# Performance work log

Measured on AMD Instinct MI355X. Metric: run time of the kernel, lower is better.

## Reference

```python
import jax, jax.numpy as jnp
import numpy as np

B, S, IN, OUT, H, M = 16, 512, 512, 512, 8, 4
HF = OUT // H  # head_feats = 64


def setup_inputs() -> dict:
    key = jax.random.key(0)
    ks = jax.random.split(key, 12)
    std = 0.02
    queries = jax.random.normal(ks[0], (B, S, IN), jnp.float32)
    keys = jax.random.normal(ks[1], (B, S, IN), jnp.float32)
    timespans = jax.random.uniform(ks[2], (B, S), jnp.float32)
    # causal mask tiled over heads*batch, matching [H*B, S, S] score shape
    attention_masks = jnp.broadcast_to(jnp.tril(jnp.ones((S, S), jnp.float32)), (H * B, S, S))
    event_marks = jax.random.uniform(ks[3], (H * B, 1, S, M), jnp.float32)
    Wq = std * jax.random.normal(ks[4], (IN, OUT), jnp.float32)
    Wk = std * jax.random.normal(ks[5], (IN, OUT), jnp.float32)
    Wv = std * jax.random.normal(ks[6], (IN, OUT), jnp.float32)
    Wt = std * jax.random.normal(ks[7], (IN, OUT), jnp.float32)
    Wi = std * jax.random.normal(ks[8], (HF + 1, M * HF), jnp.float32)  # fc_i weight
    bi = jnp.zeros((M * HF,), jnp.float32)                               # fc_i bias
    weight_i = std * jax.random.normal(ks[9], (M, HF), jnp.float32)
    scale_i = jnp.zeros((M,), jnp.float32)
    return {"queries": queries, "keys": keys, "timespans": timespans,
            "attention_masks": attention_masks, "event_marks": event_marks,
            "Wq": Wq, "Wk": Wk, "Wv": Wv, "Wt": Wt, "Wi": Wi, "bi": bi,
            "weight_i": weight_i, "scale_i": scale_i}


def reference(queries, keys, timespans, attention_masks, event_marks,
              Wq, Wk, Wv, Wt, Wi, bi, weight_i, scale_i):
    # torch's cat(chunk(X, H, dim=2), dim=0) == [B,S,H,HF] -> [H,B,S,HF] -> flat h*B+b
    def split_heads(X):
        return X.reshape(B, S, H, HF).transpose(2, 0, 1, 3)  # [H,B,S,HF]

    Q = split_heads(queries @ Wq)
    K = split_heads(keys @ Wk)
    V = split_heads(keys @ Wv)
    T = split_heads(keys @ Wt)

    scores = jnp.einsum('hbqf,hbkf->hbqk', Q, K) / jnp.sqrt(jnp.float32(OUT))
    mask = attention_masks.reshape(H, B, S, S)
    scores = jnp.where(mask == 0.0, jnp.float32(-2 ** 32 + 1), scores)
    attn = jax.nn.softmax(scores, axis=-1)  # [H,B,Sq,Sk]

    E = jnp.einsum('hbqk,hbkf->hbqf', attn, T)  # events fed to intensity net

    # --- Hawkes intensities ---
    ts = jnp.broadcast_to(timespans[None, :, :, None], (H, B, S, 1))
    mu = jax.nn.sigmoid(jnp.concatenate([E, ts], axis=-1) @ Wi + bi)  # [H,B,S,M*HF]
    mu = mu.reshape(H, B, S, M, HF)  # chunk over marks along feature dim
    scale = jnp.exp(scale_i)  # [M]
    lam = jnp.einsum('hbsmf,mf->hbsm', mu, weight_i) / scale
    lam = scale * jnp.log1p(jnp.exp(lam))  # scaled softplus, [H,B,S,M]

    # mark_inty[h,b,q,k] = sum_m lam[h,b,q,m] * event_marks[h,b,k,m]
    em = event_marks.reshape(H, B, S, M)
    mark_inty = jnp.einsum('hbqm,hbkm->hbqk', lam, em)

    out = jnp.einsum('hbqk,hbkf->hbqf', attn * mark_inty, V)
    out = out.transpose(1, 2, 0, 3).reshape(B, S, OUT) + queries[..., :OUT]
    all_mark_inty = lam.reshape(H * B, S, M)
    return out, all_mark_inty
```

## Files before the change

kernel.cpp:

```cpp
#include <hip/hip_runtime.h>
#include <math.h>

typedef __attribute__((ext_vector_type(8))) short short8;
typedef __attribute__((ext_vector_type(4))) float f32x4;

static __device__ __forceinline__ unsigned short f2bf(float f) {
  unsigned int u = __float_as_uint(f);
  u += 0x7FFFu + ((u >> 16) & 1u);
  return (unsigned short)(u >> 16);
}

static __device__ __forceinline__ void cp16(void* lds, const void* g) {
  __builtin_amdgcn_global_load_lds((const __attribute__((address_space(1))) void*)g,
                                   (__attribute__((address_space(3))) void*)lds,
                                   16, 0, 0);
}

__global__ __launch_bounds__(256) void convert_k(
    const float* __restrict__ qin, const float* __restrict__ kin,
    const float* __restrict__ Wq, const float* __restrict__ Wk,
    const float* __restrict__ Wv, const float* __restrict__ Wt,
    const float* __restrict__ Wi,
    unsigned short* __restrict__ qbf, unsigned short* __restrict__ kbf,
    unsigned short* __restrict__ Wb, unsigned short* __restrict__ WiF)
{
  __shared__ unsigned short tr[64 * 68];
  const int blk = blockIdx.x, tid = threadIdx.x;
  if (blk < 8192) {
    const float* src = (blk < 4096) ? qin : kin;
    unsigned short* dst = (blk < 4096) ? qbf : kbf;
    int i = ((blk & 4095) * 256 + tid) * 4;
    float4 v = *(const float4*)(src + i);
    ushort4 o;
    o.x = f2bf(v.x); o.y = f2bf(v.y); o.z = f2bf(v.z); o.w = f2bf(v.w);
    *(ushort4*)(dst + i) = o;
  } else if (blk < 8448) {
    int t = blk - 8192;
    int which = t >> 6, tile = t & 63;
    int r0 = (tile >> 3) << 6, c0 = (tile & 7) << 6;
    const float* W = (which == 0) ? Wq : (which == 1) ? Wk : (which == 2) ? Wv : Wt;
    const int rr = tid >> 4, cc = (tid & 15) << 2;
#pragma unroll
    for (int u = 0; u < 4; ++u) {
      int r = rr + u * 16;
      float4 v = *(const float4*)(W + (size_t)(r0 + r) * 512 + c0 + cc);
      tr[(cc + 0) * 68 + r] = f2bf(v.x);
      tr[(cc + 1) * 68 + r] = f2bf(v.y);
      tr[(cc + 2) * 68 + r] = f2bf(v.z);
      tr[(cc + 3) * 68 + r] = f2bf(v.w);
    }
    __syncthreads();
    unsigned short* dst = Wb + which * 262144;
#pragma unroll
    for (int u = 0; u < 4; ++u) {
      int c = rr + u * 16;
      ushort4 o = *(const ushort4*)&tr[c * 68 + cc];
      *(ushort4*)(dst + (size_t)(c0 + c) * 512 + r0 + cc) = o;
    }
  } else {
    int e = (blk - 8448) * 256 + tid;
    int j = e & 7, ll = (e >> 3) & 63, r = e >> 9;
    int kk = r % 3, nt = r / 3;
    int col = nt * 16 + (ll & 15);
    int k = kk * 32 + (ll >> 4) * 8 + j;
    float val = (k < 64) ? Wi[k * 256 + col] : ((k == 64) ? Wi[16384 + col] : 0.0f);
    WiF[e] = f2bf(val);
  }
}

__global__ __launch_bounds__(256) void proj_mfma(
    const unsigned short* __restrict__ qin_bf, const unsigned short* __restrict__ kin_bf,
    const unsigned short* __restrict__ Wb,
    unsigned short* __restrict__ Qg, unsigned short* __restrict__ Kg,
    unsigned short* __restrict__ Vt, unsigned short* __restrict__ Tt)
{
  const int which = blockIdx.z;
  const unsigned short* A = (which == 0) ? qin_bf : kin_bf;
  const unsigned short* W = Wb + which * 262144;
  const int row0 = blockIdx.x * 128;
  const int col0 = blockIdx.y * 128;
  const int tid = threadIdx.x;
  const int wv = tid >> 6, l = tid & 63;
  const int quad = l >> 4, lc = l & 15;
  const int wm = wv >> 1, wn = wv & 1;

  __shared__ unsigned short Asm[128 * 32];
  __shared__ unsigned short Bsm[128 * 32];

  f32x4 acc[4][4] = {};
  const int c0 = tid, c1 = tid + 256;

  for (int k0 = 0; k0 < 512; k0 += 32) {
    __syncthreads();
    cp16(&Asm[c0 * 8], A + (size_t)(row0 + (c0 >> 2)) * 512 + k0 + (c0 & 3) * 8);
    cp16(&Asm[c1 * 8], A + (size_t)(row0 + (c1 >> 2)) * 512 + k0 + (c1 & 3) * 8);
    cp16(&Bsm[c0 * 8], W + (size_t)(col0 + (c0 >> 2)) * 512 + k0 + (c0 & 3) * 8);
    cp16(&Bsm[c1 * 8], W + (size_t)(col0 + (c1 >> 2)) * 512 + k0 + (c1 & 3) * 8);
    __syncthreads();
    short8 a[4], b[4];
#pragma unroll
    for (int mi = 0; mi < 4; ++mi)
      a[mi] = *(const short8*)&Asm[(wm * 64 + mi * 16 + lc) * 32 + quad * 8];
#pragma unroll
    for (int nj = 0; nj < 4; ++nj)
      b[nj] = *(const short8*)&Bsm[(wn * 64 + nj * 16 + lc) * 32 + quad * 8];
#pragma unroll
    for (int mi = 0; mi < 4; ++mi)
#pragma unroll
      for (int nj = 0; nj < 4; ++nj)
        acc[mi][nj] = __builtin_amdgcn_mfma_f32_16x16x32_bf16(a[mi], b[nj], acc[mi][nj], 0, 0, 0);
  }

  const int h = (col0 >> 6) + wn;
  const int bidx = row0 >> 9;
  const int hb = h * 16 + bidx;
  if (which < 2) {
    unsigned short* C = (which == 0) ? Qg : Kg;
#pragma unroll
    for (int mi = 0; mi < 4; ++mi) {
      int sbase = (row0 & 511) + wm * 64 + mi * 16 + quad * 4;
#pragma unroll
      for (int nj = 0; nj < 4; ++nj) {
        size_t base = (size_t)hb * 32768 + (size_t)sbase * 64 + nj * 16 + lc;
#pragma unroll
        for (int reg = 0; reg < 4; ++reg)
          C[base + (size_t)reg * 64] = f2bf(acc[mi][nj][reg]);
      }
    }
  } else {
    unsigned short* C = (which == 2) ? Vt : Tt;
    unsigned short* scr = wn ? Bsm : Asm;
    const int sb = (row0 & 511) + wm * 64;
    __syncthreads();
#pragma unroll
    for (int round = 0; round < 2; ++round) {
      if (wm == round) {
#pragma unroll
        for (int mi = 0; mi < 4; ++mi)
#pragma unroll
          for (int nj = 0; nj < 4; ++nj)
#pragma unroll
            for (int reg = 0; reg < 4; ++reg) {
              int f = nj * 16 + lc, s = mi * 16 + quad * 4 + reg;
              int g = (s >> 3) ^ (f & 7);
              scr[f * 64 + g * 8 + (s & 7)] = f2bf(acc[mi][nj][reg]);
            }
#pragma unroll
        for (int it = 0; it < 8; ++it) {
          int fl = it * 8 + (l >> 3);
          int gg = (l & 7) ^ (fl & 7);
          short8 v = *(const short8*)&scr[fl * 64 + gg * 8];
          *(short8*)(C + (size_t)hb * 32768 + (size_t)fl * 512 + sb + (l & 7) * 8) = v;
        }
      }
      __syncthreads();
    }
  }
}

__global__ __launch_bounds__(256, 3) void attn_fused(
    const unsigned short* __restrict__ Qg, const unsigned short* __restrict__ Kg,
    const unsigned short* __restrict__ Vtg, const unsigned short* __restrict__ Ttg,
    const unsigned short* __restrict__ WiF,
    const float* __restrict__ bi, const float* __restrict__ wim,
    const float* __restrict__ sci, const float* __restrict__ tsp,
    const float* __restrict__ em, const float* __restrict__ queries,
    float* __restrict__ out, float* __restrict__ lamout)
{
  const int hb = blockIdx.y;
  const int qt = 7 - blockIdx.x;
  const int q0 = qt << 6;
  const int tid = threadIdx.x, wv = tid >> 6, l = tid & 63;
  const int quad = l >> 4, lc = l & 15;
  const int xg = lc & 7;

  __shared__ unsigned short Qs[4096];
  __shared__ unsigned short Ks[4096];
  __shared__ unsigned short TVs[4096];
  __shared__ unsigned short Wl[4][1536];
  __shared__ float emS[256];

  const int e1 = tid + 256;
  const int sr0 = tid >> 3, sg0 = (tid & 7) ^ (sr0 & 7);
  const int sr1 = e1 >> 3,  sg1 = (e1 & 7) ^ (sr1 & 7);
  const int sqk0 = sr0 * 64 + sg0 * 8,  sqk1 = sr1 * 64 + sg1 * 8;
  const int stv0 = sr0 * 512 + sg0 * 8, stv1 = sr1 * 512 + sg1 * 8;

  const float scl = 0.044194173824159216f;
  const int gqbase = q0 + wv * 16 + quad * 4;

  const unsigned short* Qbase = Qg + (size_t)hb * 32768 + q0 * 64;
  cp16(&Qs[tid * 8], Qbase + sqk0);
  cp16(&Qs[e1 * 8], Qbase + sqk1);

  f32x4 Eacc[4] = {};
  float lsum[4] = {0.f, 0.f, 0.f, 0.f};

  for (int kt = 0; kt <= qt; ++kt) {
    const int k0 = kt << 6;
    __syncthreads();
    const unsigned short* Kbase = Kg + (size_t)hb * 32768 + k0 * 64;
    cp16(&Ks[tid * 8], Kbase + sqk0);
    cp16(&Ks[e1 * 8], Kbase + sqk1);
    const unsigned short* Tbase = Ttg + (size_t)hb * 32768 + k0;
    cp16(&TVs[tid * 8], Tbase + stv0);
    cp16(&TVs[e1 * 8], Tbase + stv1);
    __syncthreads();

    f32x4 sc[4] = {};
#pragma unroll
    for (int kk = 0; kk < 2; ++kk) {
      short8 a = *(const short8*)&Qs[(wv * 16 + lc) * 64 + ((kk * 4 + quad) ^ xg) * 8];
#pragma unroll
      for (int nj = 0; nj < 4; ++nj) {
        short8 b = *(const short8*)&Ks[(nj * 16 + lc) * 64 + ((kk * 4 + quad) ^ xg) * 8];
        sc[nj] = __builtin_amdgcn_mfma_f32_16x16x32_bf16(a, b, sc[nj], 0, 0, 0);
      }
    }
    const bool diag = (kt == qt);
#pragma unroll
    for (int nj = 0; nj < 4; ++nj) {
      int col = nj * 16 + lc;
#pragma unroll
      for (int reg = 0; reg < 4; ++reg) {
        float pv = __expf(sc[nj][reg] * scl);
        if (diag && (k0 + col) > (gqbase + reg)) pv = 0.0f;
        lsum[reg] += pv;
        int row = quad * 4 + reg;
        int gp = (nj * 2 + (lc >> 3)) ^ (row & 7);
        Wl[wv][row * 96 + gp * 8 + (lc & 7)] = f2bf(pv);
      }
    }
#pragma unroll
    for (int kk = 0; kk < 2; ++kk) {
      short8 a = *(const short8*)&Wl[wv][lc * 96 + ((kk * 4 + quad) ^ xg) * 8];
#pragma unroll
      for (int fj = 0; fj < 4; ++fj) {
        short8 b = *(const short8*)&TVs[(fj * 16 + lc) * 64 + ((kk * 4 + quad) ^ xg) * 8];
        Eacc[fj] = __builtin_amdgcn_mfma_f32_16x16x32_bf16(a, b, Eacc[fj], 0, 0, 0);
      }
    }
  }

  float inv[4];
#pragma unroll
  for (int reg = 0; reg < 4; ++reg) {
    float s = lsum[reg];
#pragma unroll
    for (int off = 1; off < 16; off <<= 1) s += __shfl_xor(s, off);
    inv[reg] = 1.0f / s;
  }

#pragma unroll
  for (int reg = 0; reg < 4; ++reg) {
    int row = quad * 4 + reg;
    unsigned short* rp = &Wl[wv][row * 96];
#pragma unroll
    for (int fj = 0; fj < 4; ++fj) {
      int gp = (fj * 2 + (lc >> 3)) ^ (row & 7);
      rp[gp * 8 + (lc & 7)] = f2bf(Eacc[fj][reg] * inv[reg]);
    }
    float tsv = (lc == 0) ? tsp[(hb & 15) * 512 + gqbase + reg] : 0.0f;
    int gt = 8 + ((lc >> 3) ^ (row & 3));
    rp[gt * 8 + (lc & 7)] = f2bf(tsv);
    int gz = 8 + ((2 + (lc >> 3)) ^ (row & 3));
    rp[gz * 8 + (lc & 7)] = 0;
  }

  short8 ia[3];
  ia[0] = *(const short8*)&Wl[wv][lc * 96 + ((0 + quad) ^ xg) * 8];
  ia[1] = *(const short8*)&Wl[wv][lc * 96 + ((4 + quad) ^ xg) * 8];
  ia[2] = *(const short8*)&Wl[wv][lc * 96 + (8 + (quad ^ (lc & 3))) * 8];
  float lam4[4][4] = {};
#pragma unroll
  for (int nt = 0; nt < 16; ++nt) {
    f32x4 iacc = {};
#pragma unroll
    for (int kk = 0; kk < 3; ++kk) {
      short8 b = *(const short8*)(WiF + ((nt * 3 + kk) * 64 + l) * 8);
      iacc = __builtin_amdgcn_mfma_f32_16x16x32_bf16(ia[kk], b, iacc, 0, 0, 0);
    }
    float bvv = bi[nt * 16 + lc];
    float wmv = wim[nt * 16 + lc];
#pragma unroll
    for (int reg = 0; reg < 4; ++reg) {
      float mu = 1.0f / (1.0f + __expf(-(iacc[reg] + bvv)));
      lam4[reg][nt >> 2] += mu * wmv;
    }
  }
#pragma unroll
  for (int m = 0; m < 4; ++m) {
    float scv = __expf(sci[m]);
#pragma unroll
    for (int reg = 0; reg < 4; ++reg) {
      float s = lam4[reg][m];
#pragma unroll
      for (int off = 1; off < 16; off <<= 1) s += __shfl_xor(s, off);
      float z = s / scv;
      float sp = (z > 20.0f) ? z : log1pf(__expf(z));
      lam4[reg][m] = scv * sp;
    }
  }
  if (lc < 4) {
#pragma unroll
    for (int reg = 0; reg < 4; ++reg) {
      float v = (lc == 0) ? lam4[reg][0] : (lc == 1) ? lam4[reg][1]
              : (lc == 2) ? lam4[reg][2] : lam4[reg][3];
      lamout[((size_t)hb * 512 + gqbase + reg) * 4 + lc] = v;
    }
  }

  f32x4 Oacc[4] = {};
  for (int kt = 0; kt <= qt; ++kt) {
    const int k0 = kt << 6;
    __syncthreads();
    const unsigned short* Kbase = Kg + (size_t)hb * 32768 + k0 * 64;
    cp16(&Ks[tid * 8], Kbase + sqk0);
    cp16(&Ks[e1 * 8], Kbase + sqk1);
    const unsigned short* Vbase = Vtg + (size_t)hb * 32768 + k0;
    cp16(&TVs[tid * 8], Vbase + stv0);
    cp16(&TVs[e1 * 8], Vbase + stv1);
    emS[tid] = em[(size_t)hb * 2048 + k0 * 4 + tid];
    __syncthreads();

    f32x4 sc[4] = {};
#pragma unroll
    for (int kk = 0; kk < 2; ++kk) {
      short8 a = *(const short8*)&Qs[(wv * 16 + lc) * 64 + ((kk * 4 + quad) ^ xg) * 8];
#pragma unroll
      for (int nj = 0; nj < 4; ++nj) {
        short8 b = *(const short8*)&Ks[(nj * 16 + lc) * 64 + ((kk * 4 + quad) ^ xg) * 8];
        sc[nj] = __builtin_amdgcn_mfma_f32_16x16x32_bf16(a, b, sc[nj], 0, 0, 0);
      }
    }
    const bool diag = (kt == qt);
#pragma unroll
    for (int nj = 0; nj < 4; ++nj) {
      int col = nj * 16 + lc;
      float4 emv = *(const float4*)&emS[col * 4];
#pragma unroll
      for (int reg = 0; reg < 4; ++reg) {
        float pv = (diag && (k0 + col) > (gqbase + reg))
                       ? 0.0f : __expf(sc[nj][reg] * scl) * inv[reg];
        float mk = lam4[reg][0] * emv.x + lam4[reg][1] * emv.y +
                   lam4[reg][2] * emv.z + lam4[reg][3] * emv.w;
        int row = quad * 4 + reg;
        int gp = (nj * 2 + (lc >> 3)) ^ (row & 7);
        Wl[wv][row * 96 + gp * 8 + (lc & 7)] = f2bf(pv * mk);
      }
    }
#pragma unroll
    for (int kk = 0; kk < 2; ++kk) {
      short8 a = *(const short8*)&Wl[wv][lc * 96 + ((kk * 4 + quad) ^ xg) * 8];
#pragma unroll
      for (int fj = 0; fj < 4; ++fj) {
        short8 b = *(const short8*)&TVs[(fj * 16 + lc) * 64 + ((kk * 4 + quad) ^ xg) * 8];
        Oacc[fj] = __builtin_amdgcn_mfma_f32_16x16x32_bf16(a, b, Oacc[fj], 0, 0, 0);
      }
    }
  }

  const int h = hb >> 4, bidx = hb & 15;
#pragma unroll
  for (int reg = 0; reg < 4; ++reg) {
    size_t o = (size_t)bidx * 262144 + (size_t)(gqbase + reg) * 512 + h * 64 + lc;
#pragma unroll
    for (int fj = 0; fj < 4; ++fj)
      out[o + fj * 16] = Oacc[fj][reg] + queries[o + fj * 16];
  }
}

extern "C" void kernel_launch(void* const* d_in, const int* in_sizes, int n_in,
                              void* d_out, int out_size, void* d_ws, size_t ws_size,
                              hipStream_t stream)
{
  (void)in_sizes; (void)n_in; (void)out_size; (void)ws_size;
  const float* queries = (const float*)d_in[0];
  const float* keys    = (const float*)d_in[1];
  const float* tsp     = (const float*)d_in[2];
  const float* em      = (const float*)d_in[4];
  const float* Wq      = (const float*)d_in[5];
  const float* Wk      = (const float*)d_in[6];
  const float* Wv      = (const float*)d_in[7];
  const float* Wt      = (const float*)d_in[8];
  const float* Wi      = (const float*)d_in[9];
  const float* bi      = (const float*)d_in[10];
  const float* wim     = (const float*)d_in[11];
  const float* sci     = (const float*)d_in[12];
  float* out = (float*)d_out;

  char* w = (char*)d_ws;
  unsigned short* Qg     = (unsigned short*)(w + 0);
  unsigned short* Kg     = (unsigned short*)(w + 8388608);
  unsigned short* Vt     = (unsigned short*)(w + 16777216);
  unsigned short* Tt     = (unsigned short*)(w + 25165824);
  unsigned short* qin_bf = (unsigned short*)(w + 33554432);
  unsigned short* kin_bf = (unsigned short*)(w + 41943040);
  unsigned short* Wb     = (unsigned short*)(w + 50331648);
  unsigned short* WiF    = (unsigned short*)(w + 52428800);

  convert_k<<<8544, 256, 0, stream>>>(queries, keys, Wq, Wk, Wv, Wt, Wi,
                                      qin_bf, kin_bf, Wb, WiF);
  proj_mfma<<<dim3(64, 4, 4), 256, 0, stream>>>(qin_bf, kin_bf, Wb, Qg, Kg, Vt, Tt);
  attn_fused<<<dim3(8, 128), 256, 0, stream>>>(Qg, Kg, Vt, Tt, WiF, bi, wim, sci,
                                               tsp, em, queries, out,
                                               out + 4194304);
}
```

Before: 323.8 us.

## Factor mark intensity through per-mark scaled V to drop second attention pass

Since lam depends only on the query row, the attn*mark_inty product is factored as sum_m lam[q,m] * (attn @ (em[:,m]*V)). A new kernel precomputes four mark-scaled copies of V in bf16, and the fused kernel accumulates all four in the same key loop as E, so the second QK^T/softmax pass is gone. Each block also handles a pair of query tiles (qt and 7-qt) to balance causal work, with grid halved and occupancy hint lowered. The cost is four times the V traffic and LDS, many more accumulator registers, and an extra pre-pass kernel with a larger workspace.

New measurement: 357.4 us. 1.1x slower.

```diff
diff --git a/kernel.cpp b/kernel.cpp
--- a/kernel.cpp
+++ b/kernel.cpp
@@ -8,6 +8,9 @@
   unsigned int u = __float_as_uint(f);
   u += 0x7FFFu + ((u >> 16) & 1u);
   return (unsigned short)(u >> 16);
+}
+static __device__ __forceinline__ float bf2f(unsigned short u) {
+  return __uint_as_float(((unsigned int)u) << 16);
 }
 
 static __device__ __forceinline__ void cp16(void* lds, const void* g) {
@@ -158,27 +161,50 @@
   }
 }
 
-__global__ __launch_bounds__(256, 3) void attn_fused(
+__global__ __launch_bounds__(256) void vm_scale(
+    const unsigned short* __restrict__ Vt, const float* __restrict__ em,
+    unsigned short* __restrict__ Vm)
+{
+  const int hb = blockIdx.x >> 3, f0 = (blockIdx.x & 7) * 8;
+  const int s = threadIdx.x * 2;
+  float4 e0 = *(const float4*)(em + ((size_t)hb * 512 + s) * 4);
+  float4 e1 = *(const float4*)(em + ((size_t)hb * 512 + s + 1) * 4);
+  float em0[4] = {e0.x, e0.y, e0.z, e0.w};
+  float em1[4] = {e1.x, e1.y, e1.z, e1.w};
+#pragma unroll
+  for (int f = 0; f < 8; ++f) {
+    unsigned int v = *(const unsigned int*)(Vt + (size_t)hb * 32768 + (size_t)(f0 + f) * 512 + s);
+    float v0 = bf2f((unsigned short)(v & 0xFFFF));
+    float v1 = bf2f((unsigned short)(v >> 16));
+#pragma unroll
+    for (int m = 0; m < 4; ++m) {
+      unsigned int o = (unsigned int)f2bf(v0 * em0[m]) |
+                       ((unsigned int)f2bf(v1 * em1[m]) << 16);
+      *(unsigned int*)(Vm + (size_t)hb * 131072 + (size_t)m * 32768 +
+                       (size_t)(f0 + f) * 512 + s) = o;
+    }
+  }
+}
+
+__global__ __launch_bounds__(256, 2) void attn_fused(
     const unsigned short* __restrict__ Qg, const unsigned short* __restrict__ Kg,
-    const unsigned short* __restrict__ Vtg, const unsigned short* __restrict__ Ttg,
+    const unsigned short* __restrict__ Ttg, const unsigned short* __restrict__ Vmg,
     const unsigned short* __restrict__ WiF,
     const float* __restrict__ bi, const float* __restrict__ wim,
     const float* __restrict__ sci, const float* __restrict__ tsp,
-    const float* __restrict__ em, const float* __restrict__ queries,
+    const float* __restrict__ queries,
     float* __restrict__ out, float* __restrict__ lamout)
 {
   const int hb = blockIdx.y;
-  const int qt = 7 - blockIdx.x;
-  const int q0 = qt << 6;
   const int tid = threadIdx.x, wv = tid >> 6, l = tid & 63;
   const int quad = l >> 4, lc = l & 15;
   const int xg = lc & 7;
 
   __shared__ unsigned short Qs[4096];
   __shared__ unsigned short Ks[4096];
-  __shared__ unsigned short TVs[4096];
+  __shared__ unsigned short Ts[4096];
+  __shared__ unsigned short Vms[4][4096];
   __shared__ unsigned short Wl[4][1536];
-  __shared__ float emS[256];
 
   const int e1 = tid + 256;
   const int sr0 = tid >> 3, sg0 = (tid & 7) ^ (sr0 & 7);
@@ -187,186 +213,163 @@
   const int stv0 = sr0 * 512 + sg0 * 8, stv1 = sr1 * 512 + sg1 * 8;
 
   const float scl = 0.044194173824159216f;
-  const int gqbase = q0 + wv * 16 + quad * 4;
-
-  const unsigned short* Qbase = Qg + (size_t)hb * 32768 + q0 * 64;
-  cp16(&Qs[tid * 8], Qbase + sqk0);
-  cp16(&Qs[e1 * 8], Qbase + sqk1);
-
-  f32x4 Eacc[4] = {};
-  float lsum[4] = {0.f, 0.f, 0.f, 0.f};
-
-  for (int kt = 0; kt <= qt; ++kt) {
-    const int k0 = kt << 6;
-    __syncthreads();
-    const unsigned short* Kbase = Kg + (size_t)hb * 32768 + k0 * 64;
-    cp16(&Ks[tid * 8], Kbase + sqk0);
-    cp16(&Ks[e1 * 8], Kbase + sqk1);
-    const unsigned short* Tbase = Ttg + (size_t)hb * 32768 + k0;
-    cp16(&TVs[tid * 8], Tbase + stv0);
-    cp16(&TVs[e1 * 8], Tbase + stv1);
-    __syncthreads();
-
-    f32x4 sc[4] = {};
-#pragma unroll
-    for (int kk = 0; kk < 2; ++kk) {
-      short8 a = *(const short8*)&Qs[(wv * 16 + lc) * 64 + ((kk * 4 + quad) ^ xg) * 8];
+
+  for (int half = 0; half < 2; ++half) {
+    const int qt = half ? (7 - blockIdx.x) : blockIdx.x;
+    const int q0 = qt << 6;
+    const int gqbase = q0 + wv * 16 + quad * 4;
+    __syncthreads();
+    const unsigned short* Qbase = Qg + (size_t)hb * 32768 + q0 * 64;
+    cp16(&Qs[tid * 8], Qbase + sqk0);
+    cp16(&Qs[e1 * 8], Qbase + sqk1);
+    __syncthreads();
+    short8 aq[2];
+    aq[0] = *(const short8*)&Qs[(wv * 16 + lc) * 64 + ((0 + quad) ^ xg) * 8];
+    aq[1] = *(const short8*)&Qs[(wv * 16 + lc) * 64 + ((4 + quad) ^ xg) * 8];
+
+    f32x4 Eacc[4] = {};
+    f32x4 U[4][4] = {};
+    float lsum[4] = {0.f, 0.f, 0.f, 0.f};
+
+    for (int kt = 0; kt <= qt; ++kt) {
+      const int k0 = kt << 6;
+      __syncthreads();
+      const unsigned short* Kbase = Kg + (size_t)hb * 32768 + k0 * 64;
+      cp16(&Ks[tid * 8], Kbase + sqk0);
+      cp16(&Ks[e1 * 8], Kbase + sqk1);
+      const unsigned short* Tbase = Ttg + (size_t)hb * 32768 + k0;
+      cp16(&Ts[tid * 8], Tbase + stv0);
+      cp16(&Ts[e1 * 8], Tbase + stv1);
+#pragma unroll
+      for (int m = 0; m < 4; ++m) {
+        const unsigned short* Vbase = Vmg + (size_t)hb * 131072 + (size_t)m * 32768 + k0;
+        cp16(&Vms[m][tid * 8], Vbase + stv0);
+        cp16(&Vms[m][e1 * 8], Vbase + stv1);
+      }
+      __syncthreads();
+
+      f32x4 sc[4] = {};
+#pragma unroll
+      for (int kk = 0; kk < 2; ++kk)
+#pragma unroll
+        for (int nj = 0; nj < 4; ++nj) {
+          short8 b = *(const short8*)&Ks[(nj * 16 + lc) * 64 + ((kk * 4 + quad) ^ xg) * 8];
+          sc[nj] = __builtin_amdgcn_mfma_f32_16x16x32_bf16(aq[kk], b, sc[nj], 0, 0, 0);
+        }
+      const bool diag = (kt == qt);
 #pragma unroll
       for (int nj = 0; nj < 4; ++nj) {
-        short8 b = *(const short8*)&Ks[(nj * 16 + lc) * 64 + ((kk * 4 + quad) ^ xg) * 8];
-        sc[nj] = __builtin_amdgcn_mfma_f32_16x16x32_bf16(a, b, sc[nj], 0, 0, 0);
-      }
-    }
-    const bool diag = (kt == qt);
-#pragma unroll
-    for (int nj = 0; nj < 4; ++nj) {
-      int col = nj * 16 + lc;
+        int col = nj * 16 + lc;
+#pragma unroll
+        for (int reg = 0; reg < 4; ++reg) {
+          float pv = __expf(sc[nj][reg] * scl);
+          if (diag && (k0 + col) > (gqbase + reg)) pv = 0.0f;
+          lsum[reg] += pv;
+          int row = quad * 4 + reg;
+          int gp = (nj * 2 + (lc >> 3)) ^ (row & 7);
+          Wl[wv][row * 96 + gp * 8 + (lc & 7)] = f2bf(pv);
+        }
+      }
+      short8 ap[2];
+      ap[0] = *(const short8*)&Wl[wv][lc * 96 + ((0 + quad) ^ xg) * 8];
+      ap[1] = *(const short8*)&Wl[wv][lc * 96 + ((4 + quad) ^ xg) * 8];
+#pragma unroll
+      for (int kk = 0; kk < 2; ++kk)
+#pragma unroll
+        for (int fj = 0; fj < 4; ++fj) {
+          short8 b = *(const short8*)&Ts[(fj * 16 + lc) * 64 + ((kk * 4 + quad) ^ xg) * 8];
+          Eacc[fj] = __builtin_amdgcn_mfma_f32_16x16x32_bf16(ap[kk], b, Eacc[fj], 0, 0, 0);
+        }
+#pragma unroll
+      for (int m = 0; m < 4; ++m)
+#pragma unroll
+        for (int kk = 0; kk < 2; ++kk)
+#pragma unroll
+          for (int fj = 0; fj < 4; ++fj) {
+            short8 b = *(const short8*)&Vms[m][(fj * 16 + lc) * 64 + ((kk * 4 + quad) ^ xg) * 8];
+            U[m][fj] = __builtin_amdgcn_mfma_f32_16x16x32_bf16(ap[kk], b, U[m][fj], 0, 0, 0);
+          }
+    }
+
+    float inv[4];
+#pragma unroll
+    for (int reg = 0; reg < 4; ++reg) {
+      float s = lsum[reg];
+#pragma unroll
+      for (int off = 1; off < 16; off <<= 1) s += __shfl_xor(s, off);
+      inv[reg] = 1.0f / s;
+    }
+
+#pragma unroll
+    for (int reg = 0; reg < 4; ++reg) {
+      int row = quad * 4 + reg;
+      unsigned short* rp = &Wl[wv][row * 96];
+#pragma unroll
+      for (int fj = 0; fj < 4; ++fj) {
+        int gp = (fj * 2 + (lc >> 3)) ^ (row & 7);
+        rp[gp * 8 + (lc & 7)] = f2bf(Eacc[fj][reg] * inv[reg]);
+      }
+      float tsv = (lc == 0) ? tsp[(hb & 15) * 512 + gqbase + reg] : 0.0f;
+      int gt = 8 + ((lc >> 3) ^ (row & 3));
+      rp[gt * 8 + (lc & 7)] = f2bf(tsv);
+      int gz = 8 + ((2 + (lc >> 3)) ^ (row & 3));
+      rp[gz * 8 + (lc & 7)] = 0;
+    }
+
+    short8 ia[3];
+    ia[0] = *(const short8*)&Wl[wv][lc * 96 + ((0 + quad) ^ xg) * 8];
+    ia[1] = *(const short8*)&Wl[wv][lc * 96 + ((4 + quad) ^ xg) * 8];
+    ia[2] = *(const short8*)&Wl[wv][lc * 96 + (8 + (quad ^ (lc & 3))) * 8];
+    float lam4[4][4] = {};
+#pragma unroll
+    for (int nt = 0; nt < 16; ++nt) {
+      f32x4 iacc = {};
+#pragma unroll
+      for (int kk = 0; kk < 3; ++kk) {
+        short8 b = *(const short8*)(WiF + ((nt * 3 + kk) * 64 + l) * 8);
+        iacc = __builtin_amdgcn_mfma_f32_16x16x32_bf16(ia[kk], b, iacc, 0, 0, 0);
+      }
+      float bvv = bi[nt * 16 + lc];
+      float wmv = wim[nt * 16 + lc];
 #pragma unroll
       for (int reg = 0; reg < 4; ++reg) {
-        float pv = __expf(sc[nj][reg] * scl);
-        if (diag && (k0 + col) > (gqbase + reg)) pv = 0.0f;
-        lsum[reg] += pv;
-        int row = quad * 4 + reg;
-        int gp = (nj * 2 + (lc >> 3)) ^ (row & 7);
-        Wl[wv][row * 96 + gp * 8 + (lc & 7)] = f2bf(pv);
-      }
-    }
-#pragma unroll
-    for (int kk = 0; kk < 2; ++kk) {
-      short8 a = *(const short8*)&Wl[wv][lc * 96 + ((kk * 4 + quad) ^ xg) * 8];
+        float mu = 1.0f / (1.0f + __expf(-(iacc[reg] + bvv)));
+        lam4[reg][nt >> 2] += mu * wmv;
+      }
+    }
+#pragma unroll
+    for (int m = 0; m < 4; ++m) {
+      float scv = __expf(sci[m]);
+#pragma unroll
+      for (int reg = 0; reg < 4; ++reg) {
+        float s = lam4[reg][m];
+#pragma unroll
+        for (int off = 1; off < 16; off <<= 1) s += __shfl_xor(s, off);
+        float z = s / scv;
+        float sp = (z > 20.0f) ? z : log1pf(__expf(z));
+        lam4[reg][m] = scv * sp;
+      }
+    }
+    if (lc < 4) {
+#pragma unroll
+      for (int reg = 0; reg < 4; ++reg) {
+        float v = (lc == 0) ? lam4[reg][0] : (lc == 1) ? lam4[reg][1]
+                : (lc == 2) ? lam4[reg][2] : lam4[reg][3];
+        lamout[((size_t)hb * 512 + gqbase + reg) * 4 + lc] = v;
+      }
+    }
+
+    const int h = hb >> 4, bidx = hb & 15;
+#pragma unroll
+    for (int reg = 0; reg < 4; ++reg) {
+      size_t o = (size_t)bidx * 262144 + (size_t)(gqbase + reg) * 512 + h * 64 + lc;
 #pragma unroll
       for (int fj = 0; fj < 4; ++fj) {
-        short8 b = *(const short8*)&TVs[(fj * 16 + lc) * 64 + ((kk * 4 + quad) ^ xg) * 8];
-        Eacc[fj] = __builtin_amdgcn_mfma_f32_16x16x32_bf16(a, b, Eacc[fj], 0, 0, 0);
-      }
-    }
-  }
-
-  float inv[4];
-#pragma unroll
-  for (int reg = 0; reg < 4; ++reg) {
-    float s = lsum[reg];
-#pragma unroll
-    for (int off = 1; off < 16; off <<= 1) s += __shfl_xor(s, off);
-    inv[reg] = 1.0f / s;
-  }
-
-#pragma unroll
-  for (int reg = 0; reg < 4; ++reg) {
-    int row = quad * 4 + reg;
-    unsigned short* rp = &Wl[wv][row * 96];
-#pragma unroll
-    for (int fj = 0; fj < 4; ++fj) {
-      int gp = (fj * 2 + (lc >> 3)) ^ (row & 7);
-      rp[gp * 8 + (lc & 7)] = f2bf(Eacc[fj][reg] * inv[reg]);
-    }
-    float tsv = (lc == 0) ? tsp[(hb & 15) * 512 + gqbase + reg] : 0.0f;
-    int gt = 8 + ((lc >> 3) ^ (row & 3));
-    rp[gt * 8 + (lc & 7)] = f2bf(tsv);
-    int gz = 8 + ((2 + (lc >> 3)) ^ (row & 3));
-    rp[gz * 8 + (lc & 7)] = 0;
-  }
-
-  short8 ia[3];
-  ia[0] = *(const short8*)&Wl[wv][lc * 96 + ((0 + quad) ^ xg) * 8];
-  ia[1] = *(const short8*)&Wl[wv][lc * 96 + ((4 + quad) ^ xg) * 8];
-  ia[2] = *(const short8*)&Wl[wv][lc * 96 + (8 + (quad ^ (lc & 3))) * 8];
-  float lam4[4][4] = {};
-#pragma unroll
-  for (int nt = 0; nt < 16; ++nt) {
-    f32x4 iacc = {};
-#pragma unroll
-    for (int kk = 0; kk < 3; ++kk) {
-      short8 b = *(const short8*)(WiF + ((nt * 3 + kk) * 64 + l) * 8);
-      iacc = __builtin_amdgcn_mfma_f32_16x16x32_bf16(ia[kk], b, iacc, 0, 0, 0);
-    }
-    float bvv = bi[nt * 16 + lc];
-    float wmv = wim[nt * 16 + lc];
-#pragma unroll
-    for (int reg = 0; reg < 4; ++reg) {
-      float mu = 1.0f / (1.0f + __expf(-(iacc[reg] + bvv)));
-      lam4[reg][nt >> 2] += mu * wmv;
-    }
-  }
-#pragma unroll
-  for (int m = 0; m < 4; ++m) {
-    float scv = __expf(sci[m]);
-#pragma unroll
-    for (int reg = 0; reg < 4; ++reg) {
-      float s = lam4[reg][m];
-#pragma unroll
-      for (int off = 1; off < 16; off <<= 1) s += __shfl_xor(s, off);
-      float z = s / scv;
-      float sp = (z > 20.0f) ? z : log1pf(__expf(z));
-      lam4[reg][m] = scv * sp;
-    }
-  }
-  if (lc < 4) {
-#pragma unroll
-    for (int reg = 0; reg < 4; ++reg) {
-      float v = (lc == 0) ? lam4[reg][0] : (lc == 1) ? lam4[reg][1]
-              : (lc == 2) ? lam4[reg][2] : lam4[reg][3];
-      lamout[((size_t)hb * 512 + gqbase + reg) * 4 + lc] = v;
-    }
-  }
-
-  f32x4 Oacc[4] = {};
-  for (int kt = 0; kt <= qt; ++kt) {
-    const int k0 = kt << 6;
-    __syncthreads();
-    const unsigned short* Kbase = Kg + (size_t)hb * 32768 + k0 * 64;
-    cp16(&Ks[tid * 8], Kbase + sqk0);
-    cp16(&Ks[e1 * 8], Kbase + sqk1);
-    const unsigned short* Vbase = Vtg + (size_t)hb * 32768 + k0;
-    cp16(&TVs[tid * 8], Vbase + stv0);
-    cp16(&TVs[e1 * 8], Vbase + stv1);
-    emS[tid] = em[(size_t)hb * 2048 + k0 * 4 + tid];
-    __syncthreads();
-
-    f32x4 sc[4] = {};
-#pragma unroll
-    for (int kk = 0; kk < 2; ++kk) {
-      short8 a = *(const short8*)&Qs[(wv * 16 + lc) * 64 + ((kk * 4 + quad) ^ xg) * 8];
-#pragma unroll
-      for (int nj = 0; nj < 4; ++nj) {
-        short8 b = *(const short8*)&Ks[(nj * 16 + lc) * 64 + ((kk * 4 + quad) ^ xg) * 8];
-        sc[nj] = __builtin_amdgcn_mfma_f32_16x16x32_bf16(a, b, sc[nj], 0, 0, 0);
-      }
-    }
-    const bool diag = (kt == qt);
-#pragma unroll
-    for (int nj = 0; nj < 4; ++nj) {
-      int col = nj * 16 + lc;
-      float4 emv = *(const float4*)&emS[col * 4];
-#pragma unroll
-      for (int reg = 0; reg < 4; ++reg) {
-        float pv = (diag && (k0 + col) > (gqbase + reg))
-                       ? 0.0f : __expf(sc[nj][reg] * scl) * inv[reg];
-        float mk = lam4[reg][0] * emv.x + lam4[reg][1] * emv.y +
-                   lam4[reg][2] * emv.z + lam4[reg][3] * emv.w;
-        int row = quad * 4 + reg;
-        int gp = (nj * 2 + (lc >> 3)) ^ (row & 7);
-        Wl[wv][row * 96 + gp * 8 + (lc & 7)] = f2bf(pv * mk);
-      }
-    }
-#pragma unroll
-    for (int kk = 0; kk < 2; ++kk) {
-      short8 a = *(const short8*)&Wl[wv][lc * 96 + ((kk * 4 + quad) ^ xg) * 8];
-#pragma unroll
-      for (int fj = 0; fj < 4; ++fj) {
-        short8 b = *(const short8*)&TVs[(fj * 16 + lc) * 64 + ((kk * 4 + quad) ^ xg) * 8];
-        Oacc[fj] = __builtin_amdgcn_mfma_f32_16x16x32_bf16(a, b, Oacc[fj], 0, 0, 0);
-      }
-    }
-  }
-
-  const int h = hb >> 4, bidx = hb & 15;
-#pragma unroll
-  for (int reg = 0; reg < 4; ++reg) {
-    size_t o = (size_t)bidx * 262144 + (size_t)(gqbase + reg) * 512 + h * 64 + lc;
-#pragma unroll
-    for (int fj = 0; fj < 4; ++fj)
-      out[o + fj * 16] = Oacc[fj][reg] + queries[o + fj * 16];
+        float acc = lam4[reg][0] * U[0][fj][reg] + lam4[reg][1] * U[1][fj][reg] +
+                    lam4[reg][2] * U[2][fj][reg] + lam4[reg][3] * U[3][fj][reg];
+        out[o + fj * 16] = acc * inv[reg] + queries[o + fj * 16];
+      }
+    }
   }
 }
 
@@ -394,15 +397,16 @@
   unsigned short* Kg     = (unsigned short*)(w + 8388608);
   unsigned short* Vt     = (unsigned short*)(w + 16777216);
   unsigned short* Tt     = (unsigned short*)(w + 25165824);
-  unsigned short* qin_bf = (unsigned short*)(w + 33554432);
-  unsigned short* kin_bf = (unsigned short*)(w + 41943040);
-  unsigned short* Wb     = (unsigned short*)(w + 50331648);
-  unsigned short* WiF    = (unsigned short*)(w + 52428800);
+  unsigned short* Vm     = (unsigned short*)(w + 33554432);
+  unsigned short* qin_bf = (unsigned short*)(w + 67108864);
+  unsigned short* kin_bf = (unsigned short*)(w + 75497472);
+  unsigned short* Wb     = (unsigned short*)(w + 83886080);
+  unsigned short* WiF    = (unsigned short*)(w + 85983232);
 
   convert_k<<<8544, 256, 0, stream>>>(queries, keys, Wq, Wk, Wv, Wt, Wi,
                                       qin_bf, kin_bf, Wb, WiF);
   proj_mfma<<<dim3(64, 4, 4), 256, 0, stream>>>(qin_bf, kin_bf, Wb, Qg, Kg, Vt, Tt);
-  attn_fused<<<dim3(8, 128), 256, 0, stream>>>(Qg, Kg, Vt, Tt, WiF, bi, wim, sci,
-                                               tsp, em, queries, out,
-                                               out + 4194304);
-}
+  vm_scale<<<1024, 256, 0, stream>>>(Vt, em, Vm);
+  attn_fused<<<dim3(4, 128), 256, 0, stream>>>(Qg, Kg, Tt, Vm, WiF, bi, wim, sci,
+                                               tsp, queries, out, out + 4194304);
+}
```
